# Kernel optimization log

Hardware: AMD Instinct MI355X
Metric: run time of the kernel (lower is better)

The kernel has to match this reference:

```python
import jax, jax.numpy as jnp
from jax import lax
import numpy as np


def setup_inputs() -> dict:
    key = jax.random.key(0)
    kx, kw = jax.random.split(key)
    x = jax.random.normal(kx, (128, 512, 512), dtype=jnp.float32)  # [B, H, W]
    w = jax.random.normal(kw, (7, 7), dtype=jnp.float32)           # [k, k]
    return {"x": x, "w": w}


def reference(x, w):
    # Original: pad input by (k-1)//2 on each spatial side, then 'valid'
    # cross-correlation with the [k,k] kernel -> 'same' output [B, H, W].
    # lax.conv_general_dilated performs cross-correlation, matching
    # sum_{u,v} w[u,v] * x[i+u, j+v].
    k = w.shape[0]
    pad = (k - 1) // 2
    lhs = x[:, None, :, :]          # [B, 1, H, W]  (NCHW)
    rhs = w[None, None, :, :]       # [1, 1, k, k]  (OIHW)
    out = lax.conv_general_dilated(
        lhs, rhs,
        window_strides=(1, 1),
        padding=[(pad, pad), (pad, pad)],
        dimension_numbers=("NCHW", "OIHW", "NCHW"),
    )
    return out[:, 0, :, :]          # [B, H, W]
```

## Files before the change

### kernel.cpp

```cpp
#include <hip/hip_runtime.h>

typedef short  bf16x8 __attribute__((ext_vector_type(8)));
typedef float  f32x4  __attribute__((ext_vector_type(4)));

#define LSTR  72
#define LROWS 70
#define NCHK  18
#define CHT   (LROWS * NCHK)
#define NTILE 4
#define TSZ   (LROWS * LSTR)
#define TPAD  8

static __device__ __forceinline__ unsigned int rne16(float f) {
    unsigned int u = __float_as_uint(f);
    return (u + 0x7FFFu + ((u >> 16) & 1u)) >> 16;
}

__global__ void build_bfrag(const float* __restrict__ w, bf16x8* __restrict__ ws) {
    const int l   = threadIdx.x;
    const int l15 = l & 15;
    const int u0  = (l >> 4) * 8;
#pragma unroll
    for (int dy = 0; dy < 7; ++dy) {
        union { unsigned int u[4]; bf16x8 v; } bb;
#pragma unroll
        for (int qp = 0; qp < 4; ++qp) {
            unsigned int half[2];
#pragma unroll
            for (int h = 0; h < 2; ++h) {
                const int d = u0 + qp * 2 + h - l15 - 1;
                const float val = (d >= 0 && d < 7) ? w[dy * 7 + d] : 0.f;
                half[h] = rne16(val);
            }
            bb.u[qp] = half[0] | (half[1] << 16);
        }
        ws[dy * 64 + l] = bb.v;
    }
}

__global__ __launch_bounds__(256)
void conv7x7_mfma(const float* __restrict__ x, const bf16x8* __restrict__ Bws,
                  float* __restrict__ out) {
    __shared__ unsigned short tile[2][TSZ + TPAD];

    const int W = 512, H = 512;
    const int raw = blockIdx.x;
    const int bi  = (raw & 7) * 256 + (raw >> 3);
    const int n   = bi >> 4;
    const int ty  = (bi >> 1) & 7;
    const int g   = bi & 1;
    const int y0  = ty * 64;
    const int x0g = g * 256;

    const float* xn = x + (size_t)n * (H * W);
    float*       on = out + (size_t)n * (H * W);

    const int t   = threadIdx.x;
    const int l   = t & 63;
    const int wv  = t >> 6;
    const int l15 = l & 15;
    const int lk  = l >> 4;
    const int u0  = lk * 8;

    if (t < TPAD) { tile[0][TSZ + t] = 0; tile[1][TSZ + t] = 0; }

    bf16x8 Bf[7];
#pragma unroll
    for (int dy = 0; dy < 7; ++dy) Bf[dy] = Bws[dy * 64 + l];

    int  d_roff[5], d_loff[5], d_xoff[5];
    bool d_rok[5], d_on[5];
#pragma unroll
    for (int it = 0; it < 5; ++it) {
        const int idx = t + 256 * it;
        const int r   = idx / NCHK;
        const int cc  = idx - r * NCHK;
        const int gr  = y0 - 3 + r;
        d_on[it]   = (idx < CHT);
        d_rok[it]  = (idx < CHT) && (gr >= 0) && (gr < H);
        d_xoff[it] = x0g - 4 + 4 * cc;
        d_roff[it] = gr * W;
        d_loff[it] = r * LSTR + 4 * cc;
    }

    float4 sreg[5];

#define ISSUE(k_)                                                              \
    {                                                                          \
        _Pragma("unroll")                                                      \
        for (int it = 0; it < 5; ++it) {                                       \
            const int gc = d_xoff[it] + 64 * (k_);                             \
            float4 v = make_float4(0.f, 0.f, 0.f, 0.f);                        \
            if (d_rok[it] && gc >= 0 && gc <= W - 4)                           \
                v = *reinterpret_cast<const float4*>(&xn[d_roff[it] + gc]);    \
            sreg[it] = v;                                                      \
        }                                                                      \
    }

#define LDSWRITE(buf_)                                                         \
    {                                                                          \
        _Pragma("unroll")                                                      \
        for (int it = 0; it < 5; ++it) {                                       \
            if (d_on[it]) {                                                    \
                const unsigned p0 = rne16(sreg[it].x) | (rne16(sreg[it].y) << 16); \
                const unsigned p1 = rne16(sreg[it].z) | (rne16(sreg[it].w) << 16); \
                *reinterpret_cast<uint2*>(&tile[buf_][d_loff[it]]) =           \
                    make_uint2(p0, p1);                                        \
            }                                                                  \
        }                                                                      \
    }

    ISSUE(0)

#pragma unroll
    for (int k = 0; k < NTILE; ++k) {
        LDSWRITE(k & 1)
        __syncthreads();
        if (k + 1 < NTILE) ISSUE(k + 1)

        const int xk = x0g + 64 * k;
#pragma unroll
        for (int jo = 0; jo < 4; ++jo) {
            f32x4 acc = {0.f, 0.f, 0.f, 0.f};
#pragma unroll
            for (int dy = 0; dy < 7; ++dy) {
                const int row = wv * 16 + l15 + dy;
                const bf16x8 a = *reinterpret_cast<const bf16x8*>(
                    &tile[k & 1][row * LSTR + jo * 16 + u0]);
                acc = __builtin_amdgcn_mfma_f32_16x16x32_bf16(a, Bf[dy], acc,
                                                              0, 0, 0);
            }
#pragma unroll
            for (int rr = 0; rr < 4; ++rr) {
                const int gr = y0 + wv * 16 + lk * 4 + rr;
                on[(size_t)gr * W + xk + jo * 16 + l15] = acc[rr];
            }
        }
    }

#undef ISSUE
#undef LDSWRITE
}

extern "C" void kernel_launch(void* const* d_in, const int* in_sizes, int n_in,
                              void* d_out, int out_size, void* d_ws, size_t ws_size,
                              hipStream_t stream) {
    const float* x = (const float*)d_in[0];
    const float* w = (const float*)d_in[1];
    float* out = (float*)d_out;
    bf16x8* bws = (bf16x8*)d_ws;

    build_bfrag<<<1, 64, 0, stream>>>(w, bws);

    const int nblocks = 128 * 8 * 2;
    conv7x7_mfma<<<nblocks, 256, 0, stream>>>(x, bws, out);
}
```

Measured before the change: 58.40 us.

## Give each wave a private LDS halo tile and prefetch two tiles ahead

Each wave now loads and converts its own 22-row halo strip into a private double-buffered LDS region. This removes the block-wide __syncthreads between the global-to-LDS stage and the MFMA compute. The tile loop is unrolled with two register staging sets, so global loads for the next two column tiles are in flight while the current one is computed. In exchange, the halo rows are re-read by every wave, which adds global and L2 traffic, and the extra staging registers plus the larger LDS footprint raise per-block resource use.

```diff
diff --git a/kernel.cpp b/kernel.cpp
--- a/kernel.cpp
+++ b/kernel.cpp
@@ -3,13 +3,13 @@
 typedef short  bf16x8 __attribute__((ext_vector_type(8)));
 typedef float  f32x4  __attribute__((ext_vector_type(4)));
 
-#define LSTR  72
-#define LROWS 70
-#define NCHK  18
-#define CHT   (LROWS * NCHK)
+#define WROWS 22
+#define WSTR  72
+#define WPAD  8
+#define WSZ   (WROWS * WSTR + WPAD)
+#define NCHW  18
+#define CHTW  (WROWS * NCHW)
 #define NTILE 4
-#define TSZ   (LROWS * LSTR)
-#define TPAD  8
 
 static __device__ __forceinline__ unsigned int rne16(float f) {
     unsigned int u = __float_as_uint(f);
@@ -41,7 +41,7 @@
 __global__ __launch_bounds__(256)
 void conv7x7_mfma(const float* __restrict__ x, const bf16x8* __restrict__ Bws,
                   float* __restrict__ out) {
-    __shared__ unsigned short tile[2][TSZ + TPAD];
+    __shared__ unsigned short lds[4][2][WSZ];
 
     const int W = 512, H = 512;
     const int raw = blockIdx.x;
@@ -49,8 +49,6 @@
     const int n   = bi >> 4;
     const int ty  = (bi >> 1) & 7;
     const int g   = bi & 1;
-    const int y0  = ty * 64;
-    const int x0g = g * 256;
 
     const float* xn = x + (size_t)n * (H * W);
     float*       on = out + (size_t)n * (H * W);
@@ -62,84 +60,95 @@
     const int lk  = l >> 4;
     const int u0  = lk * 8;
 
-    if (t < TPAD) { tile[0][TSZ + t] = 0; tile[1][TSZ + t] = 0; }
+    const int y0  = ty * 64 + wv * 16;
+    const int x0g = g * 256;
+
+    if (l < WPAD) { lds[wv][0][WROWS * WSTR + l] = 0; lds[wv][1][WROWS * WSTR + l] = 0; }
 
     bf16x8 Bf[7];
 #pragma unroll
     for (int dy = 0; dy < 7; ++dy) Bf[dy] = Bws[dy * 64 + l];
 
-    int  d_roff[5], d_loff[5], d_xoff[5];
-    bool d_rok[5], d_on[5];
+    int  d_roff[7], d_loff[7], d_xoff[7];
+    bool d_rok[7], d_act[7];
 #pragma unroll
-    for (int it = 0; it < 5; ++it) {
-        const int idx = t + 256 * it;
-        const int r   = idx / NCHK;
-        const int cc  = idx - r * NCHK;
+    for (int it = 0; it < 7; ++it) {
+        const int idx = l + 64 * it;
+        const int r   = idx / NCHW;
+        const int cc  = idx - r * NCHW;
         const int gr  = y0 - 3 + r;
-        d_on[it]   = (idx < CHT);
-        d_rok[it]  = (idx < CHT) && (gr >= 0) && (gr < H);
+        d_act[it]  = (idx < CHTW);
+        d_rok[it]  = d_act[it] && (gr >= 0) && (gr < H);
         d_xoff[it] = x0g - 4 + 4 * cc;
         d_roff[it] = gr * W;
-        d_loff[it] = r * LSTR + 4 * cc;
+        d_loff[it] = r * WSTR + 4 * cc;
     }
 
-    float4 sreg[5];
+    float4 sregA[7], sregB[7];
 
-#define ISSUE(k_)                                                              \
+#define ISSUE(SR, k_)                                                          \
     {                                                                          \
         _Pragma("unroll")                                                      \
-        for (int it = 0; it < 5; ++it) {                                       \
+        for (int it = 0; it < 7; ++it) {                                       \
             const int gc = d_xoff[it] + 64 * (k_);                             \
             float4 v = make_float4(0.f, 0.f, 0.f, 0.f);                        \
             if (d_rok[it] && gc >= 0 && gc <= W - 4)                           \
                 v = *reinterpret_cast<const float4*>(&xn[d_roff[it] + gc]);    \
-            sreg[it] = v;                                                      \
+            SR[it] = v;                                                        \
         }                                                                      \
     }
 
-#define LDSWRITE(buf_)                                                         \
+#define LDSWRITE(SR, buf_)                                                     \
     {                                                                          \
         _Pragma("unroll")                                                      \
-        for (int it = 0; it < 5; ++it) {                                       \
-            if (d_on[it]) {                                                    \
-                const unsigned p0 = rne16(sreg[it].x) | (rne16(sreg[it].y) << 16); \
-                const unsigned p1 = rne16(sreg[it].z) | (rne16(sreg[it].w) << 16); \
-                *reinterpret_cast<uint2*>(&tile[buf_][d_loff[it]]) =           \
+        for (int it = 0; it < 7; ++it) {                                       \
+            if (d_act[it]) {                                                   \
+                const unsigned p0 = rne16(SR[it].x) | (rne16(SR[it].y) << 16); \
+                const unsigned p1 = rne16(SR[it].z) | (rne16(SR[it].w) << 16); \
+                *reinterpret_cast<uint2*>(&lds[wv][buf_][d_loff[it]]) =        \
                     make_uint2(p0, p1);                                        \
             }                                                                  \
         }                                                                      \
     }
 
-    ISSUE(0)
+#define COMPUTE(k_, buf_)                                                      \
+    {                                                                          \
+        const int xk = x0g + 64 * (k_);                                        \
+        _Pragma("unroll")                                                      \
+        for (int jo = 0; jo < 4; ++jo) {                                       \
+            f32x4 acc = {0.f, 0.f, 0.f, 0.f};                                  \
+            _Pragma("unroll")                                                  \
+            for (int dy = 0; dy < 7; ++dy) {                                   \
+                const int row = l15 + dy;                                      \
+                const bf16x8 a = *reinterpret_cast<const bf16x8*>(             \
+                    &lds[wv][buf_][row * WSTR + jo * 16 + u0]);                \
+                acc = __builtin_amdgcn_mfma_f32_16x16x32_bf16(a, Bf[dy], acc,  \
+                                                              0, 0, 0);        \
+            }                                                                  \
+            _Pragma("unroll")                                                  \
+            for (int rr = 0; rr < 4; ++rr) {                                   \
+                const int gr = y0 + lk * 4 + rr;                               \
+                on[(size_t)gr * W + xk + jo * 16 + l15] = acc[rr];             \
+            }                                                                  \
+        }                                                                      \
+    }
 
-#pragma unroll
-    for (int k = 0; k < NTILE; ++k) {
-        LDSWRITE(k & 1)
-        __syncthreads();
-        if (k + 1 < NTILE) ISSUE(k + 1)
-
-        const int xk = x0g + 64 * k;
-#pragma unroll
-        for (int jo = 0; jo < 4; ++jo) {
-            f32x4 acc = {0.f, 0.f, 0.f, 0.f};
-#pragma unroll
-            for (int dy = 0; dy < 7; ++dy) {
-                const int row = wv * 16 + l15 + dy;
-                const bf16x8 a = *reinterpret_cast<const bf16x8*>(
-                    &tile[k & 1][row * LSTR + jo * 16 + u0]);
-                acc = __builtin_amdgcn_mfma_f32_16x16x32_bf16(a, Bf[dy], acc,
-                                                              0, 0, 0);
-            }
-#pragma unroll
-            for (int rr = 0; rr < 4; ++rr) {
-                const int gr = y0 + wv * 16 + lk * 4 + rr;
-                on[(size_t)gr * W + xk + jo * 16 + l15] = acc[rr];
-            }
-        }
-    }
+    ISSUE(sregA, 0)
+    ISSUE(sregB, 1)
+    LDSWRITE(sregA, 0)
+    COMPUTE(0, 0)
+    ISSUE(sregA, 2)
+    LDSWRITE(sregB, 1)
+    COMPUTE(1, 1)
+    ISSUE(sregB, 3)
+    LDSWRITE(sregA, 0)
+    COMPUTE(2, 0)
+    LDSWRITE(sregB, 1)
+    COMPUTE(3, 1)
 
 #undef ISSUE
 #undef LDSWRITE
+#undef COMPUTE
 }
 
 extern "C" void kernel_launch(void* const* d_in, const int* in_sizes, int n_in,
```

New measurement: 55.48 us. 5.0% less time.
